# Kernel tuning notes

Hardware: AMD Instinct MI355X
Metric: run time of the kernel (lower is better)

## Reference

```python
import jax, jax.numpy as jnp
import numpy as np

H = 512      # hidden_size
GH = 512     # global_hidden_size
V = 128      # VOCAB_SIZE (one-hot arg_hot width)
D = 14       # tree depth; complete binary tree
NUM_OPS = 36
N_INT = 5    # num_internal_ops
N_NODES = 2 ** (D + 1) - 1  # 32767, heap layout: node i has children 2i+1, 2i+2


def _p(key, i, shape, s=0.05):
    return jax.random.normal(jax.random.fold_in(key, i), shape, dtype=jnp.float32) * s


def setup_inputs() -> dict:
    key = jax.random.key(0)
    return {
        "tokens": jax.random.randint(jax.random.fold_in(key, 0), (N_NODES,), 0, V),
        "validity_mask": jnp.ones((NUM_OPS,), jnp.float32),
        # binary tree-LSTM (blstm): 2 children
        "W_iou_b": _p(key, 1, (V, 3 * H)), "U_iou_b": _p(key, 2, (2, H, 3 * H)), "b_iou_b": jnp.zeros((3 * H,), jnp.float32),
        "Wf_b": _p(key, 3, (V, H)), "Uf_b": _p(key, 4, (2, H, H)), "bf_b": jnp.ones((H,), jnp.float32),
        # ternary tree-LSTM (tlstm): 3 children
        "W_iou_t": _p(key, 5, (V, 3 * H)), "U_iou_t": _p(key, 6, (3, H, 3 * H)), "b_iou_t": jnp.zeros((3 * H,), jnp.float32),
        "Wf_t": _p(key, 7, (V, H)), "Uf_t": _p(key, 8, (3, H, H)), "bf_t": jnp.ones((H,), jnp.float32),
        # FFN: one h-by-h layer (ffn_complexity = h^2 * n_layers, n_layers=1)
        "ffn_W": _p(key, 9, (H, H)), "ffn_b": jnp.zeros((H,), jnp.float32),
        # global LSTM (1 layer, 1 step), torch gate order i,f,g,o
        "lstm_Wx": _p(key, 10, (H, 4 * GH)), "lstm_Wh": _p(key, 11, (GH, 4 * GH)), "lstm_b": jnp.zeros((4 * GH,), jnp.float32),
        # actor heads on concat(root_hidden, h_glob)
        "hl_W": _p(key, 12, (H + GH, 2)), "hl_b": jnp.zeros((2,), jnp.float32),
        "int_W": _p(key, 13, (H + GH, N_INT)), "int_b": jnp.zeros((N_INT,), jnp.float32),
        "act_W": _p(key, 14, (H + GH, NUM_OPS)), "act_b": jnp.zeros((NUM_OPS,), jnp.float32),
    }


def _nary_cell(x, hk, ck, W_iou, U_iou, b_iou, Wf, Uf, bf):
    # x: [n, V]; hk, ck: [n, K, H]  (K children)
    iou = x @ W_iou + jnp.einsum('nkh,khg->ng', hk, U_iou) + b_iou
    i, o, u = jnp.split(iou, 3, axis=-1)
    f = jax.nn.sigmoid((x @ Wf + bf)[:, None, :] + jnp.einsum('nkh,khg->nkg', hk, Uf))
    c = jax.nn.sigmoid(i) * jnp.tanh(u) + jnp.sum(f * ck, axis=1)
    h = jax.nn.sigmoid(o) * jnp.tanh(c)
    return h, c


def _forward(tokens, validity_mask, W_iou_b, U_iou_b, b_iou_b, Wf_b, Uf_b, bf_b,
             W_iou_t, U_iou_t, b_iou_t, Wf_t, Uf_t, bf_t, ffn_W, ffn_b,
             lstm_Wx, lstm_Wh, lstm_b, hl_W, hl_b, int_W, int_b, act_W, act_b):
    arg_hot = jax.nn.one_hot(tokens, V, dtype=jnp.float32)  # [N_NODES, V]
    h_prev = c_prev = None
    h_ab = c_ab = None
    # apply_binary_lstm over the whole tree, bottom-up, one batched cell per level
    for lvl in range(D, -1, -1):
        n = 2 ** lvl
        x = arg_hot[n - 1:2 * n - 1]  # level lvl occupies heap slots [2^l-1, 2^{l+1}-2]
        if h_prev is None:
            hk = jnp.zeros((n, 2, H), jnp.float32)  # leaves: tz children
            ck = hk
        else:
            hk = h_prev.reshape(n, 2, H)
            ck = c_prev.reshape(n, 2, H)
        h_prev, c_prev = _nary_cell(x, hk, ck, W_iou_b, U_iou_b, b_iou_b, Wf_b, Uf_b, bf_b)
        if lvl == 1:
            h_ab, c_ab = h_prev, c_prev  # root's children a, b
    # apply_ternary_lstm at depth 0: children = (self.hidden, a.hidden, b.hidden)
    hk3 = jnp.concatenate([h_prev, h_ab], axis=0)[None]  # [1, 3, H]
    ck3 = jnp.concatenate([c_prev, c_ab], axis=0)[None]
    h_root, c_root = _nary_cell(arg_hot[0:1], hk3, ck3, W_iou_t, U_iou_t, b_iou_t, Wf_t, Uf_t, bf_t)
    # apply_ffn (1 layer) then apply_global_lstm (single step from zero state)
    h_f = jnp.maximum(h_root @ ffn_W + ffn_b, 0.0)  # [1, H]
    h_g = jnp.zeros((1, GH), jnp.float32)
    c_g = h_g
    gates = h_f @ lstm_Wx + h_g @ lstm_Wh + lstm_b
    gi, gf, gg, go = jnp.split(gates, 4, axis=-1)
    c_g = jax.nn.sigmoid(gf) * c_g + jax.nn.sigmoid(gi) * jnp.tanh(gg)
    h_g = jax.nn.sigmoid(go) * jnp.tanh(c_g)
    # actor heads
    feat = jnp.concatenate([h_f, h_g], axis=-1)  # [1, H+GH]
    hl = feat @ hl_W + hl_b
    il = feat @ int_W + int_b
    el = jnp.log(validity_mask)[None, :] + feat @ (act_W * validity_mask[None, :]) + act_b * validity_mask
    return jnp.concatenate([hl, il, el], axis=-1)  # [1, 2 + N_INT + NUM_OPS]


def reference(tokens, validity_mask, W_iou_b, U_iou_b, b_iou_b, Wf_b, Uf_b, bf_b,
              W_iou_t, U_iou_t, b_iou_t, Wf_t, Uf_t, bf_t, ffn_W, ffn_b,
              lstm_Wx, lstm_Wh, lstm_b, hl_W, hl_b, int_W, int_b, act_W, act_b):
    return _forward(tokens, validity_mask, W_iou_b, U_iou_b, b_iou_b, Wf_b, Uf_b, bf_b,
                    W_iou_t, U_iou_t, b_iou_t, Wf_t, Uf_t, bf_t, ffn_W, ffn_b,
                    lstm_Wx, lstm_Wh, lstm_b, hl_W, hl_b, int_W, int_b, act_W, act_b)
```

## Files before the change

### kernel.cpp

```cpp
#include <hip/hip_runtime.h>
#include <hip/hip_bf16.h>
#include <math.h>

#define H 512
#define V 128
#define NLEAF 16384

typedef __attribute__((ext_vector_type(4))) float f32x4;
typedef __attribute__((ext_vector_type(8))) short s16x8;
typedef __attribute__((ext_vector_type(4))) unsigned short u16x4;
typedef unsigned short ushort_t;

__device__ ushort_t g_hb0[NLEAF * H];
__device__ ushort_t g_hb1[(NLEAF / 2) * H];
__device__ float    g_c0[NLEAF * H];
__device__ float    g_c1[(NLEAF / 2) * H];
__device__ ushort_t g_UiouT[3 * H * 2 * H];
__device__ ushort_t g_UfT[H * 2 * H];
__device__ ushort_t g_UiouTt[3 * H * 3 * H];
__device__ ushort_t g_UfTt[H * 3 * H];
__device__ float    g_rpart[3 * 3072];
__device__ float    g_hf[H];
__device__ float    g_gates[4 * H];

__device__ __forceinline__ float sigm(float x) { return 1.0f / (1.0f + __expf(-x)); }
__device__ __forceinline__ float ftanh(float x) {
  return 1.0f - 2.0f / (__expf(2.0f * x) + 1.0f);
}
__device__ __forceinline__ ushort_t f2bf(float x) {
  __hip_bfloat16 b = __float2bfloat16(x);
  return *reinterpret_cast<ushort_t*>(&b);
}
__device__ __forceinline__ float bf2f(ushort_t u) {
  union { unsigned int i; float f; } v; v.i = ((unsigned int)u) << 16; return v.f;
}
__device__ __forceinline__ void gload_lds16(const void* g, void* l) {
  __builtin_amdgcn_global_load_lds(
      (const __attribute__((address_space(1))) unsigned int*)g,
      (__attribute__((address_space(3))) unsigned int*)l, 16, 0, 0);
}

__global__ __launch_bounds__(256) void k_prep(
    const float* __restrict__ s0, const float* __restrict__ s1,
    const float* __restrict__ s2, const float* __restrict__ s3,
    ushort_t* __restrict__ d0, ushort_t* __restrict__ d1,
    ushort_t* __restrict__ d2, ushort_t* __restrict__ d3,
    const int* __restrict__ tokens,
    const float* __restrict__ Wiou, const float* __restrict__ biou) {
  if (blockIdx.z == 4) {
    const int total = NLEAF * 128;
    const int bid = blockIdx.y * 48 + blockIdx.x;
    for (int q = bid * 256 + threadIdx.x; q < total; q += 2304 * 256) {
      int i = q >> 7, jv = q & 127;
      int tok = tokens[(NLEAF - 1) + i];
      const f32x4* Wr = (const f32x4*)(Wiou + (size_t)tok * 1536);
      const f32x4* bv = (const f32x4*)biou;
      f32x4 wi = Wr[jv] + bv[jv];
      f32x4 wo = Wr[128 + jv] + bv[128 + jv];
      f32x4 wu = Wr[256 + jv] + bv[256 + jv];
      u16x4 hv; f32x4 cv;
      #pragma unroll
      for (int r = 0; r < 4; ++r) {
        float c = sigm(wi[r]) * ftanh(wu[r]);
        float h = sigm(wo[r]) * ftanh(c);
        cv[r] = c;
        hv[r] = f2bf(h);
      }
      *reinterpret_cast<u16x4*>(&g_hb0[(size_t)q * 4]) = hv;
      *reinterpret_cast<f32x4*>(&g_c0[(size_t)q * 4]) = cv;
    }
    return;
  }
  const float* src; ushort_t* dst; int R, Cc;
  switch (blockIdx.z) {
    case 0: src = s0; dst = d0; R = 1024; Cc = 1536; break;
    case 1: src = s1; dst = d1; R = 1024; Cc = 512; break;
    case 2: src = s2; dst = d2; R = 1536; Cc = 1536; break;
    default: src = s3; dst = d3; R = 1536; Cc = 512; break;
  }
  int bc = blockIdx.x * 32, br = blockIdx.y * 32;
  if (bc >= Cc || br >= R) return;
  __shared__ float t[32][33];
  int tx = threadIdx.x & 31, ty = threadIdx.x >> 5;
  for (int rr = ty; rr < 32; rr += 8)
    t[rr][tx] = src[(size_t)(br + rr) * Cc + bc + tx];
  __syncthreads();
  for (int rr = ty; rr < 32; rr += 8)
    dst[(size_t)(bc + rr) * R + br + tx] = f2bf(t[tx][rr]);
}

__device__ __forceinline__ void mfma_body(int lvl,
    const int* __restrict__ tokens,
    const float* __restrict__ Wiou, const float* __restrict__ biou,
    const float* __restrict__ Wf, const float* __restrict__ bf) {
  const int n = 1 << lvl;
  const int node0 = n - 1;
  const int outp = lvl & 1;
  const ushort_t* __restrict__ hprev = outp ? g_hb0 : g_hb1;
  const float* __restrict__ cprev = outp ? g_c0 : g_c1;
  ushort_t* __restrict__ hout = outp ? g_hb1 : g_hb0;
  float* __restrict__ cout = outp ? g_c1 : g_c0;

  const int orig = blockIdx.x;
  const int qch = gridDim.x >> 3;
  const int wg = (orig & 7) * qch + (orig >> 3);
  const int i0 = (wg >> 3) * 128;
  const int j0 = (wg & 7) * 64;

  const int tid = threadIdx.x;
  const int lane = tid & 63;
  const int w = tid >> 6;
  const int wry = w >> 1;
  const int cx = w & 1;

  __shared__ f32x4 smemv[3072];
  char* smem = (char*)smemv;

  const char* gp[6];
  unsigned lb[6], lstride[6];
  {
    int kb = (lane >> 4) * 16;
    #pragma unroll
    for (int q = 0; q < 6; ++q) {
      int c = w * 6 + q;
      if (c < 8) {
        int row = i0 + c * 16 + (lane & 15);
        gp[q] = (const char*)hprev + (size_t)row * 2048 + kb;
        lb[q] = c * 1024u;
        lstride[q] = 8192u;
      } else {
        int ct = c - 8;
        int col = ct * 16 + (lane & 15);
        int g = col >> 6, jj = j0 + (col & 63);
        const ushort_t* Ub = (g < 3) ? (g_UiouT + (size_t)(g * 512 + jj) * 1024)
                                     : (g_UfT + (size_t)jj * 1024);
        gp[q] = (const char*)Ub + kb;
        lb[q] = 16384u + ct * 1024u;
        lstride[q] = 16384u;
      }
    }
  }

#define STAGE(BUF)                                                   \
  {                                                                  \
    _Pragma("unroll")                                                \
    for (int q = 0; q < 6; ++q) {                                    \
      gload_lds16(gp[q], smem + lb[q] + (unsigned)(BUF) * lstride[q]); \
      gp[q] += 64;                                                   \
    }                                                                \
  }
#define WAITV(N) asm volatile("s_waitcnt vmcnt(" #N ")" ::: "memory")

  f32x4 acc[4][10];
  #pragma unroll
  for (int a = 0; a < 4; ++a)
    #pragma unroll
    for (int b = 0; b < 10; ++b) acc[a][b] = (f32x4){0.f, 0.f, 0.f, 0.f};

#define COMPUTE(FA)                                                          \
  {                                                                          \
    const char* ab = smem + buf * 8192 + wry * 4096 + lane * 16;             \
    s16x8 a0 = *(const s16x8*)(ab);                                          \
    s16x8 a1 = *(const s16x8*)(ab + 1024);                                   \
    s16x8 a2 = *(const s16x8*)(ab + 2048);                                   \
    s16x8 a3 = *(const s16x8*)(ab + 3072);                                   \
    const char* bb = smem + 16384 + buf * 16384 + cx * 2048 + lane * 16;     \
    s16x8 b0 = *(const s16x8*)(bb);                                          \
    s16x8 b1 = *(const s16x8*)(bb + 1024);                                   \
    s16x8 b2 = *(const s16x8*)(bb + 4096);                                   \
    s16x8 b3 = *(const s16x8*)(bb + 5120);                                   \
    s16x8 b4 = *(const s16x8*)(bb + 8192);                                   \
    s16x8 b5 = *(const s16x8*)(bb + 9216);                                   \
    s16x8 b6 = *(const s16x8*)(bb + 12288);                                  \
    s16x8 b7 = *(const s16x8*)(bb + 13312);                                  \
    s16x8 aa[4] = {a0, a1, a2, a3};                                          \
    _Pragma("unroll")                                                        \
    for (int rtl = 0; rtl < 4; ++rtl) {                                      \
      acc[rtl][0] = __builtin_amdgcn_mfma_f32_16x16x32_bf16(aa[rtl], b0, acc[rtl][0], 0, 0, 0); \
      acc[rtl][1] = __builtin_amdgcn_mfma_f32_16x16x32_bf16(aa[rtl], b1, acc[rtl][1], 0, 0, 0); \
      acc[rtl][2] = __builtin_amdgcn_mfma_f32_16x16x32_bf16(aa[rtl], b2, acc[rtl][2], 0, 0, 0); \
      acc[rtl][3] = __builtin_amdgcn_mfma_f32_16x16x32_bf16(aa[rtl], b3, acc[rtl][3], 0, 0, 0); \
      acc[rtl][4] = __builtin_amdgcn_mfma_f32_16x16x32_bf16(aa[rtl], b4, acc[rtl][4], 0, 0, 0); \
      acc[rtl][5] = __builtin_amdgcn_mfma_f32_16x16x32_bf16(aa[rtl], b5, acc[rtl][5], 0, 0, 0); \
      acc[rtl][FA] = __builtin_amdgcn_mfma_f32_16x16x32_bf16(aa[rtl], b6, acc[rtl][FA], 0, 0, 0); \
      acc[rtl][FA + 1] = __builtin_amdgcn_mfma_f32_16x16x32_bf16(aa[rtl], b7, acc[rtl][FA + 1], 0, 0, 0); \
    }                                                                        \
  }

  STAGE(0); STAGE(1);
  int buf = 0;
  for (int kt = 0; kt < 16; ++kt) {
    WAITV(6);
    __builtin_amdgcn_s_barrier();
    COMPUTE(6);
    __builtin_amdgcn_s_barrier();
    STAGE(buf);
    buf ^= 1;
  }
  for (int kt = 16; kt < 30; ++kt) {
    WAITV(6);
    __builtin_amdgcn_s_barrier();
    COMPUTE(8);
    __builtin_amdgcn_s_barrier();
    STAGE(buf);
    buf ^= 1;
  }
  WAITV(6); __builtin_amdgcn_s_barrier(); COMPUTE(8); buf ^= 1;
  WAITV(0); __builtin_amdgcn_s_barrier(); COMPUTE(8);
#undef COMPUTE
#undef STAGE
#undef WAITV

  const int node_c = lane >> 4;
  const int jl = lane & 15;
  #pragma unroll
  for (int t = 0; t < 2; ++t) {
    const int j = j0 + cx * 32 + t * 16 + jl;
    const float bi = biou[j], bo = biou[512 + j], bu = biou[1024 + j], bfv = bf[j];
    #pragma unroll
    for (int rtl = 0; rtl < 4; ++rtl) {
      f32x4 vi = acc[rtl][0 + t], vo = acc[rtl][2 + t], vu = acc[rtl][4 + t],
            v0 = acc[rtl][6 + t], v1 = acc[rtl][8 + t];
      const int ib = i0 + wry * 64 + rtl * 16 + node_c * 4;
      #pragma unroll
      for (int r = 0; r < 4; ++r) {
        int i = ib + r;
        int tok = tokens[node0 + i];
        const float* Wr = Wiou + (size_t)tok * 1536;
        float fpre = Wf[(size_t)tok * 512 + j] + bfv;
        float ig = vi[r] + Wr[j] + bi;
        float og = vo[r] + Wr[512 + j] + bo;
        float ug = vu[r] + Wr[1024 + j] + bu;
        float cc = sigm(ig) * ftanh(ug)
                 + sigm(fpre + v0[r]) * cprev[(size_t)(2 * i) * 512 + j]
                 + sigm(fpre + v1[r]) * cprev[(size_t)(2 * i + 1) * 512 + j];
        float hh = sigm(og) * ftanh(cc);
        hout[(size_t)i * 512 + j] = f2bf(hh);
        cout[(size_t)i * 512 + j] = cc;
      }
    }
  }
}

__global__ __launch_bounds__(256, 2) void k_mfma_top(
    const int* __restrict__ tokens,
    const float* __restrict__ Wiou, const float* __restrict__ biou,
    const float* __restrict__ Wf, const float* __restrict__ bf) {
  mfma_body(13, tokens, Wiou, biou, Wf, bf);
}
__global__ __launch_bounds__(256, 2) void k_mfma_rest(int lvl,
    const int* __restrict__ tokens,
    const float* __restrict__ Wiou, const float* __restrict__ biou,
    const float* __restrict__ Wf, const float* __restrict__ bf) {
  mfma_body(lvl, tokens, Wiou, biou, Wf, bf);
}

__global__ __launch_bounds__(256) void k_small(int lvl,
    const int* __restrict__ tokens,
    const float* __restrict__ Wiou, const float* __restrict__ biou,
    const float* __restrict__ Wf, const float* __restrict__ bf) {
  const int n = 1 << lvl;
  const int node0 = n - 1;
  const int outp = lvl & 1;
  const ushort_t* __restrict__ hprev = outp ? g_hb0 : g_hb1;
  const float* __restrict__ cprev = outp ? g_c0 : g_c1;
  ushort_t* __restrict__ hout = outp ? g_hb1 : g_hb0;
  float* __restrict__ cout = outp ? g_c1 : g_c0;

  const int i = blockIdx.y;
  const int j0 = blockIdx.x * 64;
  const int tid = threadIdx.x;
  const int g = tid >> 6;
  const int jc = tid & 63;
  const int jj = j0 + jc;

  __shared__ float hl[1024];
  __shared__ float exch[5][64];
  for (int t = tid; t < 1024; t += 256) hl[t] = bf2f(hprev[(size_t)i * 1024 + t]);
  __syncthreads();

  const ushort_t* col = (g < 3) ? (g_UiouT + (size_t)(g * 512 + jj) * 1024)
                                : (g_UfT + (size_t)jj * 1024);
  float a0 = 0.f, a1 = 0.f;
  #pragma unroll 4
  for (int k0 = 0; k0 < 512; k0 += 8) {
    s16x8 wv = *(const s16x8*)(col + k0);
    #pragma unroll
    for (int r = 0; r < 8; ++r) a0 += hl[k0 + r] * bf2f((ushort_t)wv[r]);
  }
  #pragma unroll 4
  for (int k0 = 512; k0 < 1024; k0 += 8) {
    s16x8 wv = *(const s16x8*)(col + k0);
    #pragma unroll
    for (int r = 0; r < 8; ++r) a1 += hl[k0 + r] * bf2f((ushort_t)wv[r]);
  }
  if (g < 3) exch[g][jc] = a0 + a1;
  else { exch[3][jc] = a0; exch[4][jc] = a1; }
  __syncthreads();

  if (tid < 64) {
    int j = j0 + tid;
    float ai = exch[0][tid], ao = exch[1][tid], au = exch[2][tid];
    float af0 = exch[3][tid], af1 = exch[4][tid];
    int tok = tokens[node0 + i];
    const float* Wr = Wiou + (size_t)tok * 1536;
    float fpre = Wf[(size_t)tok * 512 + j] + bf[j];
    float ig = ai + Wr[j] + biou[j];
    float og = ao + Wr[512 + j] + biou[512 + j];
    float ug = au + Wr[1024 + j] + biou[1024 + j];
    float cc = sigm(ig) * ftanh(ug)
             + sigm(fpre + af0) * cprev[(size_t)(2 * i) * 512 + j]
             + sigm(fpre + af1) * cprev[(size_t)(2 * i + 1) * 512 + j];
    float hh = sigm(og) * ftanh(cc);
    hout[(size_t)i * 512 + j] = f2bf(hh);
    cout[(size_t)i * 512 + j] = cc;
  }
}

__global__ __launch_bounds__(256) void k_root_p1() {
  const int by = blockIdx.y;
  const int tid = threadIdx.x;
  const int c = blockIdx.x * 256 + tid;

  __shared__ float hl[512];
  {
    int m0 = by * 512;
    #pragma unroll
    for (int q = 0; q < 2; ++q) {
      int t = tid + q * 256, m = m0 + t;
      hl[t] = (m < 512) ? bf2f(g_hb0[m]) : bf2f(g_hb1[m - 512]);
    }
  }
  __syncthreads();

  float acc = 0.f;
  const ushort_t* col = nullptr;
  if (c < 1536) {
    col = g_UiouTt + (size_t)c * 1536 + by * 512;
  } else {
    int v = c - 1536;
    if ((v >> 9) == by) col = g_UfTt + (size_t)(v & 511) * 1536 + by * 512;
  }
  if (col) {
    #pragma unroll 4
    for (int k0 = 0; k0 < 512; k0 += 8) {
      s16x8 wv = *(const s16x8*)(col + k0);
      #pragma unroll
      for (int r = 0; r < 8; ++r) acc += hl[k0 + r] * bf2f((ushort_t)wv[r]);
    }
  }
  g_rpart[(size_t)by * 3072 + c] = acc;
}

__global__ __launch_bounds__(512) void k_p2h1(const int* __restrict__ tokens,
    const float* __restrict__ Wiou_t, const float* __restrict__ biou_t,
    const float* __restrict__ Wf_t, const float* __restrict__ bf_t,
    const float* __restrict__ ffnW, const float* __restrict__ ffnb) {
  __shared__ float hroot[H];
  const int j = threadIdx.x;
  float ai = g_rpart[j] + g_rpart[3072 + j] + g_rpart[6144 + j];
  float ao = g_rpart[512 + j] + g_rpart[3072 + 512 + j] + g_rpart[6144 + 512 + j];
  float au = g_rpart[1024 + j] + g_rpart[3072 + 1024 + j] + g_rpart[6144 + 1024 + j];
  float f0 = g_rpart[1536 + j] + g_rpart[3072 + 1536 + j] + g_rpart[6144 + 1536 + j];
  float f1 = g_rpart[2048 + j] + g_rpart[3072 + 2048 + j] + g_rpart[6144 + 2048 + j];
  float f2 = g_rpart[2560 + j] + g_rpart[3072 + 2560 + j] + g_rpart[6144 + 2560 + j];

  int tok = tokens[0];
  float fpre = Wf_t[(size_t)tok * H + j] + bf_t[j];
  float ig = ai + Wiou_t[(size_t)tok * 3 * H + j] + biou_t[j];
  float og = ao + Wiou_t[(size_t)tok * 3 * H + H + j] + biou_t[H + j];
  float ug = au + Wiou_t[(size_t)tok * 3 * H + 2 * H + j] + biou_t[2 * H + j];
  float cc = sigm(ig) * ftanh(ug)
           + sigm(fpre + f0) * g_c0[j]
           + sigm(fpre + f1) * g_c1[j]
           + sigm(fpre + f2) * g_c1[H + j];
  hroot[j] = sigm(og) * ftanh(cc);
  __syncthreads();

  float acc = ffnb[j];
  #pragma unroll 8
  for (int m = 0; m < H; ++m) acc += hroot[m] * ffnW[m * H + j];
  g_hf[j] = fmaxf(acc, 0.0f);
}

__global__ __launch_bounds__(64) void k_head2(const float* __restrict__ Wx,
                                              const float* __restrict__ lb) {
  int idx = blockIdx.x * 64 + threadIdx.x;
  int region = idx >> 9;
  int j = idx & 511;
  int g2 = (region == 0) ? j : ((region == 1) ? 1024 + j : 1536 + j);
  float acc = lb[g2];
  #pragma unroll 8
  for (int m = 0; m < H; ++m) acc += g_hf[m] * Wx[m * 4 * H + g2];
  g_gates[g2] = acc;
}

__global__ __launch_bounds__(512) void k_head3(const float* __restrict__ vm,
    const float* __restrict__ hlW, const float* __restrict__ hlb,
    const float* __restrict__ intW, const float* __restrict__ intb,
    const float* __restrict__ actW, const float* __restrict__ actb,
    float* __restrict__ out) {
  __shared__ float feat[2 * H];
  int j = threadIdx.x;
  float ci = sigm(g_gates[j]) * ftanh(g_gates[2 * H + j]);
  float hg = sigm(g_gates[3 * H + j]) * ftanh(ci);
  feat[j] = g_hf[j];
  feat[H + j] = hg;
  __syncthreads();

  const int wv = threadIdx.x >> 6;
  const int lane = threadIdx.x & 63;
  for (int o = wv; o < 43; o += 8) {
    const float* Wc;
    int stride, colb;
    if (o < 2)       { Wc = hlW;  stride = 2;  colb = o; }
    else if (o < 7)  { Wc = intW; stride = 5;  colb = o - 2; }
    else             { Wc = actW; stride = 36; colb = o - 7; }
    float s = 0.f;
    #pragma unroll
    for (int q = 0; q < 16; ++q) {
      int m = lane + q * 64;
      s += feat[m] * Wc[(size_t)m * stride + colb];
    }
    #pragma unroll
    for (int d = 32; d >= 1; d >>= 1) s += __shfl_xor(s, d);
    if (lane == 0) {
      float res;
      if (o < 2)      res = s + hlb[o];
      else if (o < 7) res = s + intb[o - 2];
      else {
        int a = o - 7;
        float v = vm[a];
        res = __logf(v) + s * v + actb[a] * v;
      }
      out[o] = res;
    }
  }
}

extern "C" void kernel_launch(void* const* d_in, const int* in_sizes, int n_in,
                              void* d_out, int out_size, void* d_ws, size_t ws_size,
                              hipStream_t stream) {
  (void)in_sizes; (void)n_in; (void)d_ws; (void)ws_size; (void)out_size;
  const int* tokens   = (const int*)d_in[0];
  const float* vm     = (const float*)d_in[1];
  const float* Wiou_b = (const float*)d_in[2];
  const float* Uiou_b = (const float*)d_in[3];
  const float* biou_b = (const float*)d_in[4];
  const float* Wf_b   = (const float*)d_in[5];
  const float* Uf_b   = (const float*)d_in[6];
  const float* bf_b   = (const float*)d_in[7];
  const float* Wiou_t = (const float*)d_in[8];
  const float* Uiou_t = (const float*)d_in[9];
  const float* biou_t = (const float*)d_in[10];
  const float* Wf_t   = (const float*)d_in[11];
  const float* Uf_t   = (const float*)d_in[12];
  const float* bf_t   = (const float*)d_in[13];
  const float* ffnW   = (const float*)d_in[14];
  const float* ffnb   = (const float*)d_in[15];
  const float* lstmWx = (const float*)d_in[16];
  const float* lstmb  = (const float*)d_in[18];
  const float* hlW    = (const float*)d_in[19];
  const float* hlb    = (const float*)d_in[20];
  const float* intW   = (const float*)d_in[21];
  const float* intb   = (const float*)d_in[22];
  const float* actW   = (const float*)d_in[23];
  const float* actb   = (const float*)d_in[24];

  ushort_t* UiouT;  hipGetSymbolAddress((void**)&UiouT, HIP_SYMBOL(g_UiouT));
  ushort_t* UfT;    hipGetSymbolAddress((void**)&UfT, HIP_SYMBOL(g_UfT));
  ushort_t* UiouTt; hipGetSymbolAddress((void**)&UiouTt, HIP_SYMBOL(g_UiouTt));
  ushort_t* UfTt;   hipGetSymbolAddress((void**)&UfTt, HIP_SYMBOL(g_UfTt));

  k_prep<<<dim3(48, 48, 5), 256, 0, stream>>>(
      Uiou_b, Uf_b, Uiou_t, Uf_t, UiouT, UfT, UiouTt, UfTt,
      tokens, Wiou_b, biou_b);

  k_mfma_top<<<512, 256, 0, stream>>>(tokens, Wiou_b, biou_b, Wf_b, bf_b);
  for (int lvl = 12; lvl >= 8; --lvl) {
    int nb = ((1 << lvl) / 128) * 8;
    k_mfma_rest<<<nb, 256, 0, stream>>>(lvl, tokens, Wiou_b, biou_b,
                                        Wf_b, bf_b);
  }
  for (int lvl = 7; lvl >= 0; --lvl) {
    int n = 1 << lvl;
    k_small<<<dim3(8, n), 256, 0, stream>>>(lvl, tokens, Wiou_b, biou_b,
                                            Wf_b, bf_b);
  }
  k_root_p1<<<dim3(12, 3), 256, 0, stream>>>();
  k_p2h1<<<1, 512, 0, stream>>>(tokens, Wiou_t, biou_t, Wf_t, bf_t, ffnW, ffnb);
  k_head2<<<24, 64, 0, stream>>>(lstmWx, lstmb);
  k_head3<<<1, 512, 0, stream>>>(vm, hlW, hlb, intW, intb, actW, actb, (float*)d_out);
}
```

Before: 670.5 us.

## Replace leaf-state materialization with per-token lookup table and triple-buffer MFMA pipeline

Leaf hidden and cell states depend only on the token, so the code now computes a 128-entry table instead of writing 16384 leaf rows. The top MFMA level gathers its A operand directly from that table by child token, and its epilogue reads the cell state from the table the same way. Both MFMA kernels also move from two-stage to three-stage LDS buffering, raising shared memory to 72KB per block, and use a 2D grid in place of the old swizzled block index. This removes a large leaf write and re-read in exchange for gathered loads, more LDS, and possibly lower occupancy.

```diff
diff --git a/kernel.cpp b/kernel.cpp
--- a/kernel.cpp
+++ b/kernel.cpp
@@ -8,13 +8,14 @@
 
 typedef __attribute__((ext_vector_type(4))) float f32x4;
 typedef __attribute__((ext_vector_type(8))) short s16x8;
-typedef __attribute__((ext_vector_type(4))) unsigned short u16x4;
 typedef unsigned short ushort_t;
 
 __device__ ushort_t g_hb0[NLEAF * H];
 __device__ ushort_t g_hb1[(NLEAF / 2) * H];
 __device__ float    g_c0[NLEAF * H];
 __device__ float    g_c1[(NLEAF / 2) * H];
+__device__ __align__(16) ushort_t g_htab[V * H];
+__device__ __align__(16) float    g_ctab[V * H];
 __device__ ushort_t g_UiouT[3 * H * 2 * H];
 __device__ ushort_t g_UfT[H * 2 * H];
 __device__ ushort_t g_UiouTt[3 * H * 3 * H];
@@ -45,29 +46,18 @@
     const float* __restrict__ s2, const float* __restrict__ s3,
     ushort_t* __restrict__ d0, ushort_t* __restrict__ d1,
     ushort_t* __restrict__ d2, ushort_t* __restrict__ d3,
-    const int* __restrict__ tokens,
     const float* __restrict__ Wiou, const float* __restrict__ biou) {
   if (blockIdx.z == 4) {
-    const int total = NLEAF * 128;
-    const int bid = blockIdx.y * 48 + blockIdx.x;
-    for (int q = bid * 256 + threadIdx.x; q < total; q += 2304 * 256) {
-      int i = q >> 7, jv = q & 127;
-      int tok = tokens[(NLEAF - 1) + i];
-      const f32x4* Wr = (const f32x4*)(Wiou + (size_t)tok * 1536);
-      const f32x4* bv = (const f32x4*)biou;
-      f32x4 wi = Wr[jv] + bv[jv];
-      f32x4 wo = Wr[128 + jv] + bv[128 + jv];
-      f32x4 wu = Wr[256 + jv] + bv[256 + jv];
-      u16x4 hv; f32x4 cv;
-      #pragma unroll
-      for (int r = 0; r < 4; ++r) {
-        float c = sigm(wi[r]) * ftanh(wu[r]);
-        float h = sigm(wo[r]) * ftanh(c);
-        cv[r] = c;
-        hv[r] = f2bf(h);
-      }
-      *reinterpret_cast<u16x4*>(&g_hb0[(size_t)q * 4]) = hv;
-      *reinterpret_cast<f32x4*>(&g_c0[(size_t)q * 4]) = cv;
+    const int v = blockIdx.y * 48 + blockIdx.x;
+    if (v >= V) return;
+    for (int j = threadIdx.x; j < H; j += 256) {
+      float ig = Wiou[(size_t)v * 1536 + j] + biou[j];
+      float og = Wiou[(size_t)v * 1536 + 512 + j] + biou[512 + j];
+      float ug = Wiou[(size_t)v * 1536 + 1024 + j] + biou[1024 + j];
+      float c = sigm(ig) * ftanh(ug);
+      float h = sigm(og) * ftanh(c);
+      g_htab[v * H + j] = f2bf(h);
+      g_ctab[v * H + j] = c;
     }
     return;
   }
@@ -89,82 +79,14 @@
     dst[(size_t)(bc + rr) * R + br + tx] = f2bf(t[tx][rr]);
 }
 
-__device__ __forceinline__ void mfma_body(int lvl,
-    const int* __restrict__ tokens,
-    const float* __restrict__ Wiou, const float* __restrict__ biou,
-    const float* __restrict__ Wf, const float* __restrict__ bf) {
-  const int n = 1 << lvl;
-  const int node0 = n - 1;
-  const int outp = lvl & 1;
-  const ushort_t* __restrict__ hprev = outp ? g_hb0 : g_hb1;
-  const float* __restrict__ cprev = outp ? g_c0 : g_c1;
-  ushort_t* __restrict__ hout = outp ? g_hb1 : g_hb0;
-  float* __restrict__ cout = outp ? g_c1 : g_c0;
-
-  const int orig = blockIdx.x;
-  const int qch = gridDim.x >> 3;
-  const int wg = (orig & 7) * qch + (orig >> 3);
-  const int i0 = (wg >> 3) * 128;
-  const int j0 = (wg & 7) * 64;
-
-  const int tid = threadIdx.x;
-  const int lane = tid & 63;
-  const int w = tid >> 6;
-  const int wry = w >> 1;
-  const int cx = w & 1;
-
-  __shared__ f32x4 smemv[3072];
-  char* smem = (char*)smemv;
-
-  const char* gp[6];
-  unsigned lb[6], lstride[6];
-  {
-    int kb = (lane >> 4) * 16;
-    #pragma unroll
-    for (int q = 0; q < 6; ++q) {
-      int c = w * 6 + q;
-      if (c < 8) {
-        int row = i0 + c * 16 + (lane & 15);
-        gp[q] = (const char*)hprev + (size_t)row * 2048 + kb;
-        lb[q] = c * 1024u;
-        lstride[q] = 8192u;
-      } else {
-        int ct = c - 8;
-        int col = ct * 16 + (lane & 15);
-        int g = col >> 6, jj = j0 + (col & 63);
-        const ushort_t* Ub = (g < 3) ? (g_UiouT + (size_t)(g * 512 + jj) * 1024)
-                                     : (g_UfT + (size_t)jj * 1024);
-        gp[q] = (const char*)Ub + kb;
-        lb[q] = 16384u + ct * 1024u;
-        lstride[q] = 16384u;
-      }
-    }
-  }
-
-#define STAGE(BUF)                                                   \
-  {                                                                  \
-    _Pragma("unroll")                                                \
-    for (int q = 0; q < 6; ++q) {                                    \
-      gload_lds16(gp[q], smem + lb[q] + (unsigned)(BUF) * lstride[q]); \
-      gp[q] += 64;                                                   \
-    }                                                                \
-  }
-#define WAITV(N) asm volatile("s_waitcnt vmcnt(" #N ")" ::: "memory")
-
-  f32x4 acc[4][10];
-  #pragma unroll
-  for (int a = 0; a < 4; ++a)
-    #pragma unroll
-    for (int b = 0; b < 10; ++b) acc[a][b] = (f32x4){0.f, 0.f, 0.f, 0.f};
-
-#define COMPUTE(FA)                                                          \
+#define MFMA_COMPUTE(FA)                                                     \
   {                                                                          \
     const char* ab = smem + buf * 8192 + wry * 4096 + lane * 16;             \
     s16x8 a0 = *(const s16x8*)(ab);                                          \
     s16x8 a1 = *(const s16x8*)(ab + 1024);                                   \
     s16x8 a2 = *(const s16x8*)(ab + 2048);                                   \
     s16x8 a3 = *(const s16x8*)(ab + 3072);                                   \
-    const char* bb = smem + 16384 + buf * 16384 + cx * 2048 + lane * 16;     \
+    const char* bb = smem + 24576 + buf * 16384 + cx * 2048 + lane * 16;     \
     s16x8 b0 = *(const s16x8*)(bb);                                          \
     s16x8 b1 = *(const s16x8*)(bb + 1024);                                   \
     s16x8 b2 = *(const s16x8*)(bb + 4096);                                   \
@@ -186,73 +108,228 @@
       acc[rtl][FA + 1] = __builtin_amdgcn_mfma_f32_16x16x32_bf16(aa[rtl], b7, acc[rtl][FA + 1], 0, 0, 0); \
     }                                                                        \
   }
-
-  STAGE(0); STAGE(1);
-  int buf = 0;
-  for (int kt = 0; kt < 16; ++kt) {
-    WAITV(6);
-    __builtin_amdgcn_s_barrier();
-    COMPUTE(6);
-    __builtin_amdgcn_s_barrier();
-    STAGE(buf);
-    buf ^= 1;
-  }
-  for (int kt = 16; kt < 30; ++kt) {
-    WAITV(6);
-    __builtin_amdgcn_s_barrier();
-    COMPUTE(8);
-    __builtin_amdgcn_s_barrier();
-    STAGE(buf);
-    buf ^= 1;
-  }
-  WAITV(6); __builtin_amdgcn_s_barrier(); COMPUTE(8); buf ^= 1;
-  WAITV(0); __builtin_amdgcn_s_barrier(); COMPUTE(8);
-#undef COMPUTE
-#undef STAGE
-#undef WAITV
-
-  const int node_c = lane >> 4;
-  const int jl = lane & 15;
-  #pragma unroll
-  for (int t = 0; t < 2; ++t) {
-    const int j = j0 + cx * 32 + t * 16 + jl;
-    const float bi = biou[j], bo = biou[512 + j], bu = biou[1024 + j], bfv = bf[j];
-    #pragma unroll
-    for (int rtl = 0; rtl < 4; ++rtl) {
-      f32x4 vi = acc[rtl][0 + t], vo = acc[rtl][2 + t], vu = acc[rtl][4 + t],
-            v0 = acc[rtl][6 + t], v1 = acc[rtl][8 + t];
-      const int ib = i0 + wry * 64 + rtl * 16 + node_c * 4;
-      #pragma unroll
-      for (int r = 0; r < 4; ++r) {
-        int i = ib + r;
-        int tok = tokens[node0 + i];
-        const float* Wr = Wiou + (size_t)tok * 1536;
-        float fpre = Wf[(size_t)tok * 512 + j] + bfv;
-        float ig = vi[r] + Wr[j] + bi;
-        float og = vo[r] + Wr[512 + j] + bo;
-        float ug = vu[r] + Wr[1024 + j] + bu;
-        float cc = sigm(ig) * ftanh(ug)
-                 + sigm(fpre + v0[r]) * cprev[(size_t)(2 * i) * 512 + j]
-                 + sigm(fpre + v1[r]) * cprev[(size_t)(2 * i + 1) * 512 + j];
-        float hh = sigm(og) * ftanh(cc);
-        hout[(size_t)i * 512 + j] = f2bf(hh);
-        cout[(size_t)i * 512 + j] = cc;
-      }
-    }
-  }
-}
+#define WAITV(N) asm volatile("s_waitcnt vmcnt(" #N ")" ::: "memory")
+
+#define MFMA_EPILOGUE(CREAD0, CREAD1)                                        \
+  {                                                                          \
+    const int node_c = lane >> 4;                                            \
+    const int jl = lane & 15;                                                \
+    _Pragma("unroll")                                                        \
+    for (int t = 0; t < 2; ++t) {                                            \
+      const int j = j0 + cx * 32 + t * 16 + jl;                              \
+      const float bi = biou[j], bo = biou[512 + j], bu = biou[1024 + j],     \
+                  bfv = bf[j];                                               \
+      _Pragma("unroll")                                                      \
+      for (int rtl = 0; rtl < 4; ++rtl) {                                    \
+        f32x4 vi = acc[rtl][0 + t], vo = acc[rtl][2 + t],                    \
+              vu = acc[rtl][4 + t], v0 = acc[rtl][6 + t],                    \
+              v1 = acc[rtl][8 + t];                                          \
+        const int ib = i0 + wry * 64 + rtl * 16 + node_c * 4;                \
+        _Pragma("unroll")                                                    \
+        for (int r = 0; r < 4; ++r) {                                        \
+          int i = ib + r;                                                    \
+          int tok = tokens[node0 + i];                                       \
+          const float* Wr = Wiou + (size_t)tok * 1536;                       \
+          float fpre = Wf[(size_t)tok * 512 + j] + bfv;                      \
+          float ig = vi[r] + Wr[j] + bi;                                     \
+          float og = vo[r] + Wr[512 + j] + bo;                               \
+          float ug = vu[r] + Wr[1024 + j] + bu;                              \
+          float cc = sigm(ig) * ftanh(ug)                                    \
+                   + sigm(fpre + v0[r]) * (CREAD0)                           \
+                   + sigm(fpre + v1[r]) * (CREAD1);                          \
+          float hh = sigm(og) * ftanh(cc);                                   \
+          hout[(size_t)i * 512 + j] = f2bf(hh);                              \
+          cout[(size_t)i * 512 + j] = cc;                                    \
+        }                                                                    \
+      }                                                                      \
+    }                                                                        \
+  }
 
 __global__ __launch_bounds__(256, 2) void k_mfma_top(
     const int* __restrict__ tokens,
     const float* __restrict__ Wiou, const float* __restrict__ biou,
     const float* __restrict__ Wf, const float* __restrict__ bf) {
-  mfma_body(13, tokens, Wiou, biou, Wf, bf);
-}
+  const int node0 = 8191;
+  ushort_t* __restrict__ hout = g_hb1;
+  float* __restrict__ cout = g_c1;
+
+  const int i0 = blockIdx.x * 128;
+  const int j0 = blockIdx.y * 64;
+  const int tid = threadIdx.x;
+  const int lane = tid & 63;
+  const int w = tid >> 6;
+  const int wry = w >> 1;
+  const int cx = w & 1;
+
+  __shared__ f32x4 smemv[4608];
+  char* smem = (char*)smemv;
+
+  const char* p0[6]; const char* p1[6];
+  unsigned lb[6], lstr[6], mm[6];
+  {
+    int kb = (lane >> 4) * 16;
+    #pragma unroll
+    for (int q = 0; q < 6; ++q) {
+      int c = w * 6 + q;
+      if (c < 8) {
+        int row = i0 + c * 16 + (lane & 15);
+        int t0 = tokens[(NLEAF - 1) + 2 * row];
+        int t1 = tokens[(NLEAF - 1) + 2 * row + 1];
+        p0[q] = (const char*)g_htab + (size_t)t0 * 1024 + kb;
+        p1[q] = (const char*)g_htab + (size_t)t1 * 1024 + kb;
+        mm[q] = 15u;
+        lb[q] = c * 1024u;
+        lstr[q] = 8192u;
+      } else {
+        int ct = c - 8;
+        int col = ct * 16 + (lane & 15);
+        int g = col >> 6, jj = j0 + (col & 63);
+        const ushort_t* Ub = (g < 3) ? (g_UiouT + (size_t)(g * 512 + jj) * 1024)
+                                     : (g_UfT + (size_t)jj * 1024);
+        p0[q] = (const char*)Ub + kb;
+        p1[q] = p0[q];
+        mm[q] = 63u;
+        lb[q] = 24576u + ct * 1024u;
+        lstr[q] = 16384u;
+      }
+    }
+  }
+
+#define STAGE_T(BUF, SKT)                                                    \
+  {                                                                          \
+    _Pragma("unroll")                                                        \
+    for (int q = 0; q < 6; ++q) {                                            \
+      const char* src = (((SKT) >= 16) ? p1[q] : p0[q]) +                    \
+                        (((unsigned)(SKT) & mm[q]) << 6);                    \
+      gload_lds16(src, smem + lb[q] + (unsigned)(BUF) * lstr[q]);            \
+    }                                                                        \
+  }
+
+  f32x4 acc[4][10];
+  #pragma unroll
+  for (int a = 0; a < 4; ++a)
+    #pragma unroll
+    for (int b = 0; b < 10; ++b) acc[a][b] = (f32x4){0.f, 0.f, 0.f, 0.f};
+
+  STAGE_T(0, 0); STAGE_T(1, 1); STAGE_T(2, 2);
+  int buf = 0;
+  for (int kt = 0; kt < 16; ++kt) {
+    WAITV(12);
+    __builtin_amdgcn_s_barrier();
+    MFMA_COMPUTE(6);
+    __builtin_amdgcn_s_barrier();
+    STAGE_T(buf, kt + 3);
+    buf = (buf == 2) ? 0 : buf + 1;
+  }
+  for (int kt = 16; kt < 29; ++kt) {
+    WAITV(12);
+    __builtin_amdgcn_s_barrier();
+    MFMA_COMPUTE(8);
+    __builtin_amdgcn_s_barrier();
+    STAGE_T(buf, kt + 3);
+    buf = (buf == 2) ? 0 : buf + 1;
+  }
+  WAITV(12); __builtin_amdgcn_s_barrier(); MFMA_COMPUTE(8);
+  buf = (buf == 2) ? 0 : buf + 1;
+  WAITV(6);  __builtin_amdgcn_s_barrier(); MFMA_COMPUTE(8);
+  buf = (buf == 2) ? 0 : buf + 1;
+  WAITV(0);  __builtin_amdgcn_s_barrier(); MFMA_COMPUTE(8);
+#undef STAGE_T
+
+  MFMA_EPILOGUE(g_ctab[(size_t)tokens[(NLEAF - 1) + 2 * i] * 512 + j],
+                g_ctab[(size_t)tokens[(NLEAF - 1) + 2 * i + 1] * 512 + j]);
+}
+
 __global__ __launch_bounds__(256, 2) void k_mfma_rest(int lvl,
     const int* __restrict__ tokens,
     const float* __restrict__ Wiou, const float* __restrict__ biou,
     const float* __restrict__ Wf, const float* __restrict__ bf) {
-  mfma_body(lvl, tokens, Wiou, biou, Wf, bf);
+  const int n = 1 << lvl;
+  const int node0 = n - 1;
+  const int outp = lvl & 1;
+  const ushort_t* __restrict__ hprev = outp ? g_hb0 : g_hb1;
+  const float* __restrict__ cprev = outp ? g_c0 : g_c1;
+  ushort_t* __restrict__ hout = outp ? g_hb1 : g_hb0;
+  float* __restrict__ cout = outp ? g_c1 : g_c0;
+
+  const int i0 = blockIdx.x * 128;
+  const int j0 = blockIdx.y * 64;
+  const int tid = threadIdx.x;
+  const int lane = tid & 63;
+  const int w = tid >> 6;
+  const int wry = w >> 1;
+  const int cx = w & 1;
+
+  __shared__ f32x4 smemv[4608];
+  char* smem = (char*)smemv;
+
+  const char* gp[6];
+  unsigned lb[6], lstr[6];
+  {
+    int kb = (lane >> 4) * 16;
+    #pragma unroll
+    for (int q = 0; q < 6; ++q) {
+      int c = w * 6 + q;
+      if (c < 8) {
+        int row = i0 + c * 16 + (lane & 15);
+        gp[q] = (const char*)hprev + (size_t)row * 2048 + kb;
+        lb[q] = c * 1024u;
+        lstr[q] = 8192u;
+      } else {
+        int ct = c - 8;
+        int col = ct * 16 + (lane & 15);
+        int g = col >> 6, jj = j0 + (col & 63);
+        const ushort_t* Ub = (g < 3) ? (g_UiouT + (size_t)(g * 512 + jj) * 1024)
+                                     : (g_UfT + (size_t)jj * 1024);
+        gp[q] = (const char*)Ub + kb;
+        lb[q] = 24576u + ct * 1024u;
+        lstr[q] = 16384u;
+      }
+    }
+  }
+
+#define STAGE_R(BUF)                                                 \
+  {                                                                  \
+    _Pragma("unroll")                                                \
+    for (int q = 0; q < 6; ++q) {                                    \
+      gload_lds16(gp[q], smem + lb[q] + (unsigned)(BUF) * lstr[q]);  \
+      gp[q] += 64;                                                   \
+    }                                                                \
+  }
+
+  f32x4 acc[4][10];
+  #pragma unroll
+  for (int a = 0; a < 4; ++a)
+    #pragma unroll
+    for (int b = 0; b < 10; ++b) acc[a][b] = (f32x4){0.f, 0.f, 0.f, 0.f};
+
+  STAGE_R(0); STAGE_R(1); STAGE_R(2);
+  int buf = 0;
+  for (int kt = 0; kt < 16; ++kt) {
+    WAITV(12);
+    __builtin_amdgcn_s_barrier();
+    MFMA_COMPUTE(6);
+    __builtin_amdgcn_s_barrier();
+    STAGE_R(buf);
+    buf = (buf == 2) ? 0 : buf + 1;
+  }
+  for (int kt = 16; kt < 29; ++kt) {
+    WAITV(12);
+    __builtin_amdgcn_s_barrier();
+    MFMA_COMPUTE(8);
+    __builtin_amdgcn_s_barrier();
+    STAGE_R(buf);
+    buf = (buf == 2) ? 0 : buf + 1;
+  }
+  WAITV(12); __builtin_amdgcn_s_barrier(); MFMA_COMPUTE(8);
+  buf = (buf == 2) ? 0 : buf + 1;
+  WAITV(6);  __builtin_amdgcn_s_barrier(); MFMA_COMPUTE(8);
+  buf = (buf == 2) ? 0 : buf + 1;
+  WAITV(0);  __builtin_amdgcn_s_barrier(); MFMA_COMPUTE(8);
+#undef STAGE_R
+
+  MFMA_EPILOGUE(cprev[(size_t)(2 * i) * 512 + j],
+                cprev[(size_t)(2 * i + 1) * 512 + j]);
 }
 
 __global__ __launch_bounds__(256) void k_small(int lvl,
@@ -473,14 +550,14 @@
   ushort_t* UfTt;   hipGetSymbolAddress((void**)&UfTt, HIP_SYMBOL(g_UfTt));
 
   k_prep<<<dim3(48, 48, 5), 256, 0, stream>>>(
-      Uiou_b, Uf_b, Uiou_t, Uf_t, UiouT, UfT, UiouTt, UfTt,
-      tokens, Wiou_b, biou_b);
-
-  k_mfma_top<<<512, 256, 0, stream>>>(tokens, Wiou_b, biou_b, Wf_b, bf_b);
+      Uiou_b, Uf_b, Uiou_t, Uf_t, UiouT, UfT, UiouTt, UfTt, Wiou_b, biou_b);
+
+  k_mfma_top<<<dim3(64, 8), 256, 0, stream>>>(tokens, Wiou_b, biou_b,
+                                              Wf_b, bf_b);
   for (int lvl = 12; lvl >= 8; --lvl) {
-    int nb = ((1 << lvl) / 128) * 8;
-    k_mfma_rest<<<nb, 256, 0, stream>>>(lvl, tokens, Wiou_b, biou_b,
-                                        Wf_b, bf_b);
+    int gx = (1 << lvl) / 128;
+    k_mfma_rest<<<dim3(gx, 8), 256, 0, stream>>>(lvl, tokens, Wiou_b, biou_b,
+                                                 Wf_b, bf_b);
   }
   for (int lvl = 7; lvl >= 0; --lvl) {
     int n = 1 << lvl;
```

Result: faster. 584.7 us (-12.8%).

## Precompute per-token leaf states and child projections to skip level-13 GEMM

Applied to the files above, without the earlier changes.

Leaves depend only on their token, so leaf h and c are tabulated per vocabulary entry, and the children's U projections are precomputed per token (128×3584 GEMV). Level 13 then becomes a gather-and-elementwise kernel instead of a large MFMA GEMM. The MFMA kernel also moves to a 3-stage LDS pipeline with a 2D grid, and the W/bias terms are packed into one float4 table. This removes most of the largest GEMM level at the cost of extra small kernels, more LDS per block, and bf16 rounding of leaf h before the precompute.

```diff
diff --git a/kernel.cpp b/kernel.cpp
--- a/kernel.cpp
+++ b/kernel.cpp
@@ -15,6 +15,13 @@
 __device__ ushort_t g_hb1[(NLEAF / 2) * H];
 __device__ float    g_c0[NLEAF * H];
 __device__ float    g_c1[(NLEAF / 2) * H];
+__device__ __align__(16) ushort_t g_htab[V * H];
+__device__ __align__(16) float    g_ctab[V * H];
+__device__ __align__(16) float    g_Wpack[V * H * 4];
+__device__ __align__(16) float    g_Uh0[V * 3 * H];
+__device__ __align__(16) float    g_Uh1[V * 3 * H];
+__device__ __align__(16) float    g_Vf0[V * H];
+__device__ __align__(16) float    g_Vf1[V * H];
 __device__ ushort_t g_UiouT[3 * H * 2 * H];
 __device__ ushort_t g_UfT[H * 2 * H];
 __device__ ushort_t g_UiouTt[3 * H * 3 * H];
@@ -45,29 +52,22 @@
     const float* __restrict__ s2, const float* __restrict__ s3,
     ushort_t* __restrict__ d0, ushort_t* __restrict__ d1,
     ushort_t* __restrict__ d2, ushort_t* __restrict__ d3,
-    const int* __restrict__ tokens,
-    const float* __restrict__ Wiou, const float* __restrict__ biou) {
+    const float* __restrict__ Wiou, const float* __restrict__ biou,
+    const float* __restrict__ Wf, const float* __restrict__ bf) {
   if (blockIdx.z == 4) {
-    const int total = NLEAF * 128;
-    const int bid = blockIdx.y * 48 + blockIdx.x;
-    for (int q = bid * 256 + threadIdx.x; q < total; q += 2304 * 256) {
-      int i = q >> 7, jv = q & 127;
-      int tok = tokens[(NLEAF - 1) + i];
-      const f32x4* Wr = (const f32x4*)(Wiou + (size_t)tok * 1536);
-      const f32x4* bv = (const f32x4*)biou;
-      f32x4 wi = Wr[jv] + bv[jv];
-      f32x4 wo = Wr[128 + jv] + bv[128 + jv];
-      f32x4 wu = Wr[256 + jv] + bv[256 + jv];
-      u16x4 hv; f32x4 cv;
-      #pragma unroll
-      for (int r = 0; r < 4; ++r) {
-        float c = sigm(wi[r]) * ftanh(wu[r]);
-        float h = sigm(wo[r]) * ftanh(c);
-        cv[r] = c;
-        hv[r] = f2bf(h);
-      }
-      *reinterpret_cast<u16x4*>(&g_hb0[(size_t)q * 4]) = hv;
-      *reinterpret_cast<f32x4*>(&g_c0[(size_t)q * 4]) = cv;
+    const int v = blockIdx.y * 48 + blockIdx.x;
+    if (v >= V) return;
+    for (int j = threadIdx.x; j < H; j += 256) {
+      float wi = Wiou[(size_t)v * 1536 + j] + biou[j];
+      float wo = Wiou[(size_t)v * 1536 + 512 + j] + biou[512 + j];
+      float wu = Wiou[(size_t)v * 1536 + 1024 + j] + biou[1024 + j];
+      float wf = Wf[(size_t)v * 512 + j] + bf[j];
+      f32x4 wp = {wi, wo, wu, wf};
+      *reinterpret_cast<f32x4*>(&g_Wpack[((size_t)v * 512 + j) * 4]) = wp;
+      float c = sigm(wi) * ftanh(wu);
+      float h = sigm(wo) * ftanh(c);
+      g_htab[v * H + j] = f2bf(h);
+      g_ctab[v * H + j] = c;
     }
     return;
   }
@@ -89,82 +89,75 @@
     dst[(size_t)(bc + rr) * R + br + tx] = f2bf(t[tx][rr]);
 }
 
-__device__ __forceinline__ void mfma_body(int lvl,
-    const int* __restrict__ tokens,
-    const float* __restrict__ Wiou, const float* __restrict__ biou,
-    const float* __restrict__ Wf, const float* __restrict__ bf) {
-  const int n = 1 << lvl;
-  const int node0 = n - 1;
-  const int outp = lvl & 1;
-  const ushort_t* __restrict__ hprev = outp ? g_hb0 : g_hb1;
-  const float* __restrict__ cprev = outp ? g_c0 : g_c1;
-  ushort_t* __restrict__ hout = outp ? g_hb1 : g_hb0;
-  float* __restrict__ cout = outp ? g_c1 : g_c0;
-
-  const int orig = blockIdx.x;
-  const int qch = gridDim.x >> 3;
-  const int wg = (orig & 7) * qch + (orig >> 3);
-  const int i0 = (wg >> 3) * 128;
-  const int j0 = (wg & 7) * 64;
-
-  const int tid = threadIdx.x;
-  const int lane = tid & 63;
-  const int w = tid >> 6;
-  const int wry = w >> 1;
-  const int cx = w & 1;
-
-  __shared__ f32x4 smemv[3072];
-  char* smem = (char*)smemv;
-
-  const char* gp[6];
-  unsigned lb[6], lstride[6];
-  {
-    int kb = (lane >> 4) * 16;
-    #pragma unroll
-    for (int q = 0; q < 6; ++q) {
-      int c = w * 6 + q;
-      if (c < 8) {
-        int row = i0 + c * 16 + (lane & 15);
-        gp[q] = (const char*)hprev + (size_t)row * 2048 + kb;
-        lb[q] = c * 1024u;
-        lstride[q] = 8192u;
-      } else {
-        int ct = c - 8;
-        int col = ct * 16 + (lane & 15);
-        int g = col >> 6, jj = j0 + (col & 63);
-        const ushort_t* Ub = (g < 3) ? (g_UiouT + (size_t)(g * 512 + jj) * 1024)
-                                     : (g_UfT + (size_t)jj * 1024);
-        gp[q] = (const char*)Ub + kb;
-        lb[q] = 16384u + ct * 1024u;
-        lstride[q] = 16384u;
-      }
-    }
-  }
-
-#define STAGE(BUF)                                                   \
-  {                                                                  \
-    _Pragma("unroll")                                                \
-    for (int q = 0; q < 6; ++q) {                                    \
-      gload_lds16(gp[q], smem + lb[q] + (unsigned)(BUF) * lstride[q]); \
-      gp[q] += 64;                                                   \
-    }                                                                \
-  }
-#define WAITV(N) asm volatile("s_waitcnt vmcnt(" #N ")" ::: "memory")
-
-  f32x4 acc[4][10];
-  #pragma unroll
-  for (int a = 0; a < 4; ++a)
-    #pragma unroll
-    for (int b = 0; b < 10; ++b) acc[a][b] = (f32x4){0.f, 0.f, 0.f, 0.f};
-
-#define COMPUTE(FA)                                                          \
+__global__ __launch_bounds__(256) void k_uh() {
+  const int v = blockIdx.x;
+  const int c = blockIdx.y * 256 + threadIdx.x;
+  __shared__ float hl[512];
+  for (int t = threadIdx.x; t < 512; t += 256) hl[t] = bf2f(g_htab[v * 512 + t]);
+  __syncthreads();
+  const ushort_t* col; float* dst;
+  if (c < 1536)      { col = g_UiouT + (size_t)c * 1024;
+                       dst = &g_Uh0[(size_t)v * 1536 + c]; }
+  else if (c < 3072) { col = g_UiouT + (size_t)(c - 1536) * 1024 + 512;
+                       dst = &g_Uh1[(size_t)v * 1536 + (c - 1536)]; }
+  else if (c < 3584) { col = g_UfT + (size_t)(c - 3072) * 1024;
+                       dst = &g_Vf0[(size_t)v * 512 + (c - 3072)]; }
+  else               { col = g_UfT + (size_t)(c - 3584) * 1024 + 512;
+                       dst = &g_Vf1[(size_t)v * 512 + (c - 3584)]; }
+  float acc = 0.f;
+  #pragma unroll 4
+  for (int k0 = 0; k0 < 512; k0 += 8) {
+    s16x8 wv = *(const s16x8*)(col + k0);
+    #pragma unroll
+    for (int r = 0; r < 8; ++r) acc += hl[k0 + r] * bf2f((ushort_t)wv[r]);
+  }
+  *dst = acc;
+}
+
+__global__ __launch_bounds__(256) void k_top_cell(const int* __restrict__ tokens) {
+  const int total = 8192 * 128;
+  for (int q = blockIdx.x * 256 + threadIdx.x; q < total; q += gridDim.x * 256) {
+    int i = q >> 7, jv = q & 127;
+    int t0 = tokens[(NLEAF - 1) + 2 * i];
+    int t1 = tokens[(NLEAF - 1) + 2 * i + 1];
+    int tk = tokens[8191 + i];
+    const f32x4* u0 = (const f32x4*)&g_Uh0[(size_t)t0 * 1536];
+    const f32x4* u1 = (const f32x4*)&g_Uh1[(size_t)t1 * 1536];
+    f32x4 ii = u0[jv] + u1[jv];
+    f32x4 oo = u0[128 + jv] + u1[128 + jv];
+    f32x4 uu = u0[256 + jv] + u1[256 + jv];
+    f32x4 v0 = ((const f32x4*)&g_Vf0[(size_t)t0 * 512])[jv];
+    f32x4 v1 = ((const f32x4*)&g_Vf1[(size_t)t1 * 512])[jv];
+    f32x4 c0 = ((const f32x4*)&g_ctab[(size_t)t0 * 512])[jv];
+    f32x4 c1 = ((const f32x4*)&g_ctab[(size_t)t1 * 512])[jv];
+    const f32x4* wpp = (const f32x4*)g_Wpack + (size_t)tk * 512 + jv * 4;
+    u16x4 hv; f32x4 cv;
+    #pragma unroll
+    for (int r = 0; r < 4; ++r) {
+      f32x4 wp = wpp[r];
+      float ig = ii[r] + wp[0];
+      float og = oo[r] + wp[1];
+      float ug = uu[r] + wp[2];
+      float fp = wp[3];
+      float cc = sigm(ig) * ftanh(ug) + sigm(fp + v0[r]) * c0[r]
+               + sigm(fp + v1[r]) * c1[r];
+      float hh = sigm(og) * ftanh(cc);
+      cv[r] = cc;
+      hv[r] = f2bf(hh);
+    }
+    *reinterpret_cast<u16x4*>(&g_hb1[(size_t)q * 4]) = hv;
+    *reinterpret_cast<f32x4*>(&g_c1[(size_t)q * 4]) = cv;
+  }
+}
+
+#define MFMA_COMPUTE(FA)                                                     \
   {                                                                          \
     const char* ab = smem + buf * 8192 + wry * 4096 + lane * 16;             \
     s16x8 a0 = *(const s16x8*)(ab);                                          \
     s16x8 a1 = *(const s16x8*)(ab + 1024);                                   \
     s16x8 a2 = *(const s16x8*)(ab + 2048);                                   \
     s16x8 a3 = *(const s16x8*)(ab + 3072);                                   \
-    const char* bb = smem + 16384 + buf * 16384 + cx * 2048 + lane * 16;     \
+    const char* bb = smem + 24576 + buf * 16384 + cx * 2048 + lane * 16;     \
     s16x8 b0 = *(const s16x8*)(bb);                                          \
     s16x8 b1 = *(const s16x8*)(bb + 1024);                                   \
     s16x8 b2 = *(const s16x8*)(bb + 4096);                                   \
@@ -186,37 +179,99 @@
       acc[rtl][FA + 1] = __builtin_amdgcn_mfma_f32_16x16x32_bf16(aa[rtl], b7, acc[rtl][FA + 1], 0, 0, 0); \
     }                                                                        \
   }
-
-  STAGE(0); STAGE(1);
+#define WAITV(N) asm volatile("s_waitcnt vmcnt(" #N ")" ::: "memory")
+
+__global__ __launch_bounds__(256, 2) void k_mfma_rest(int lvl,
+    const int* __restrict__ tokens) {
+  const int n = 1 << lvl;
+  const int node0 = n - 1;
+  const int outp = lvl & 1;
+  const ushort_t* __restrict__ hprev = outp ? g_hb0 : g_hb1;
+  const float* __restrict__ cprev = outp ? g_c0 : g_c1;
+  ushort_t* __restrict__ hout = outp ? g_hb1 : g_hb0;
+  float* __restrict__ cout = outp ? g_c1 : g_c0;
+
+  const int i0 = blockIdx.x * 128;
+  const int j0 = blockIdx.y * 64;
+  const int tid = threadIdx.x;
+  const int lane = tid & 63;
+  const int w = tid >> 6;
+  const int wry = w >> 1;
+  const int cx = w & 1;
+
+  __shared__ f32x4 smemv[4608];
+  char* smem = (char*)smemv;
+
+  const char* gp[6];
+  unsigned lb[6], lstr[6];
+  {
+    int kb = (lane >> 4) * 16;
+    #pragma unroll
+    for (int q = 0; q < 6; ++q) {
+      int c = w * 6 + q;
+      if (c < 8) {
+        int row = i0 + c * 16 + (lane & 15);
+        gp[q] = (const char*)hprev + (size_t)row * 2048 + kb;
+        lb[q] = c * 1024u;
+        lstr[q] = 8192u;
+      } else {
+        int ct = c - 8;
+        int col = ct * 16 + (lane & 15);
+        int g = col >> 6, jj = j0 + (col & 63);
+        const ushort_t* Ub = (g < 3) ? (g_UiouT + (size_t)(g * 512 + jj) * 1024)
+                                     : (g_UfT + (size_t)jj * 1024);
+        gp[q] = (const char*)Ub + kb;
+        lb[q] = 24576u + ct * 1024u;
+        lstr[q] = 16384u;
+      }
+    }
+  }
+
+#define STAGE_R(BUF)                                                 \
+  {                                                                  \
+    _Pragma("unroll")                                                \
+    for (int q = 0; q < 6; ++q) {                                    \
+      gload_lds16(gp[q], smem + lb[q] + (unsigned)(BUF) * lstr[q]);  \
+      gp[q] += 64;                                                   \
+    }                                                                \
+  }
+
+  f32x4 acc[4][10];
+  #pragma unroll
+  for (int a = 0; a < 4; ++a)
+    #pragma unroll
+    for (int b = 0; b < 10; ++b) acc[a][b] = (f32x4){0.f, 0.f, 0.f, 0.f};
+
+  STAGE_R(0); STAGE_R(1); STAGE_R(2);
   int buf = 0;
   for (int kt = 0; kt < 16; ++kt) {
-    WAITV(6);
+    WAITV(12);
     __builtin_amdgcn_s_barrier();
-    COMPUTE(6);
+    MFMA_COMPUTE(6);
     __builtin_amdgcn_s_barrier();
-    STAGE(buf);
-    buf ^= 1;
-  }
-  for (int kt = 16; kt < 30; ++kt) {
-    WAITV(6);
+    STAGE_R(buf);
+    buf = (buf == 2) ? 0 : buf + 1;
+  }
+  for (int kt = 16; kt < 29; ++kt) {
+    WAITV(12);
     __builtin_amdgcn_s_barrier();
-    COMPUTE(8);
+    MFMA_COMPUTE(8);
     __builtin_amdgcn_s_barrier();
-    STAGE(buf);
-    buf ^= 1;
-  }
-  WAITV(6); __builtin_amdgcn_s_barrier(); COMPUTE(8); buf ^= 1;
-  WAITV(0); __builtin_amdgcn_s_barrier(); COMPUTE(8);
-#undef COMPUTE
-#undef STAGE
-#undef WAITV
+    STAGE_R(buf);
+    buf = (buf == 2) ? 0 : buf + 1;
+  }
+  WAITV(12); __builtin_amdgcn_s_barrier(); MFMA_COMPUTE(8);
+  buf = (buf == 2) ? 0 : buf + 1;
+  WAITV(6);  __builtin_amdgcn_s_barrier(); MFMA_COMPUTE(8);
+  buf = (buf == 2) ? 0 : buf + 1;
+  WAITV(0);  __builtin_amdgcn_s_barrier(); MFMA_COMPUTE(8);
+#undef STAGE_R
 
   const int node_c = lane >> 4;
   const int jl = lane & 15;
   #pragma unroll
   for (int t = 0; t < 2; ++t) {
     const int j = j0 + cx * 32 + t * 16 + jl;
-    const float bi = biou[j], bo = biou[512 + j], bu = biou[1024 + j], bfv = bf[j];
     #pragma unroll
     for (int rtl = 0; rtl < 4; ++rtl) {
       f32x4 vi = acc[rtl][0 + t], vo = acc[rtl][2 + t], vu = acc[rtl][4 + t],
@@ -226,11 +281,11 @@
       for (int r = 0; r < 4; ++r) {
         int i = ib + r;
         int tok = tokens[node0 + i];
-        const float* Wr = Wiou + (size_t)tok * 1536;
-        float fpre = Wf[(size_t)tok * 512 + j] + bfv;
-        float ig = vi[r] + Wr[j] + bi;
-        float og = vo[r] + Wr[512 + j] + bo;
-        float ug = vu[r] + Wr[1024 + j] + bu;
+        f32x4 wp = ((const f32x4*)g_Wpack)[(size_t)tok * 512 + j];
+        float ig = vi[r] + wp[0];
+        float og = vo[r] + wp[1];
+        float ug = vu[r] + wp[2];
+        float fpre = wp[3];
         float cc = sigm(ig) * ftanh(ug)
                  + sigm(fpre + v0[r]) * cprev[(size_t)(2 * i) * 512 + j]
                  + sigm(fpre + v1[r]) * cprev[(size_t)(2 * i + 1) * 512 + j];
@@ -242,23 +297,8 @@
   }
 }
 
-__global__ __launch_bounds__(256, 2) void k_mfma_top(
-    const int* __restrict__ tokens,
-    const float* __restrict__ Wiou, const float* __restrict__ biou,
-    const float* __restrict__ Wf, const float* __restrict__ bf) {
-  mfma_body(13, tokens, Wiou, biou, Wf, bf);
-}
-__global__ __launch_bounds__(256, 2) void k_mfma_rest(int lvl,
-    const int* __restrict__ tokens,
-    const float* __restrict__ Wiou, const float* __restrict__ biou,
-    const float* __restrict__ Wf, const float* __restrict__ bf) {
-  mfma_body(lvl, tokens, Wiou, biou, Wf, bf);
-}
-
 __global__ __launch_bounds__(256) void k_small(int lvl,
-    const int* __restrict__ tokens,
-    const float* __restrict__ Wiou, const float* __restrict__ biou,
-    const float* __restrict__ Wf, const float* __restrict__ bf) {
+    const int* __restrict__ tokens) {
   const int n = 1 << lvl;
   const int node0 = n - 1;
   const int outp = lvl & 1;
@@ -300,17 +340,15 @@
 
   if (tid < 64) {
     int j = j0 + tid;
-    float ai = exch[0][tid], ao = exch[1][tid], au = exch[2][tid];
-    float af0 = exch[3][tid], af1 = exch[4][tid];
     int tok = tokens[node0 + i];
-    const float* Wr = Wiou + (size_t)tok * 1536;
-    float fpre = Wf[(size_t)tok * 512 + j] + bf[j];
-    float ig = ai + Wr[j] + biou[j];
-    float og = ao + Wr[512 + j] + biou[512 + j];
-    float ug = au + Wr[1024 + j] + biou[1024 + j];
+    f32x4 wp = ((const f32x4*)g_Wpack)[(size_t)tok * 512 + j];
+    float ig = exch[0][tid] + wp[0];
+    float og = exch[1][tid] + wp[1];
+    float ug = exch[2][tid] + wp[2];
+    float fpre = wp[3];
     float cc = sigm(ig) * ftanh(ug)
-             + sigm(fpre + af0) * cprev[(size_t)(2 * i) * 512 + j]
-             + sigm(fpre + af1) * cprev[(size_t)(2 * i + 1) * 512 + j];
+             + sigm(fpre + exch[3][tid]) * cprev[(size_t)(2 * i) * 512 + j]
+             + sigm(fpre + exch[4][tid]) * cprev[(size_t)(2 * i + 1) * 512 + j];
     float hh = sigm(og) * ftanh(cc);
     hout[(size_t)i * 512 + j] = f2bf(hh);
     cout[(size_t)i * 512 + j] = cc;
@@ -474,18 +512,18 @@
 
   k_prep<<<dim3(48, 48, 5), 256, 0, stream>>>(
       Uiou_b, Uf_b, Uiou_t, Uf_t, UiouT, UfT, UiouTt, UfTt,
-      tokens, Wiou_b, biou_b);
-
-  k_mfma_top<<<512, 256, 0, stream>>>(tokens, Wiou_b, biou_b, Wf_b, bf_b);
+      Wiou_b, biou_b, Wf_b, bf_b);
+
+  k_uh<<<dim3(128, 16), 256, 0, stream>>>();
+  k_top_cell<<<2048, 256, 0, stream>>>(tokens);
+
   for (int lvl = 12; lvl >= 8; --lvl) {
-    int nb = ((1 << lvl) / 128) * 8;
-    k_mfma_rest<<<nb, 256, 0, stream>>>(lvl, tokens, Wiou_b, biou_b,
-                                        Wf_b, bf_b);
+    int gx = (1 << lvl) / 128;
+    k_mfma_rest<<<dim3(gx, 8), 256, 0, stream>>>(lvl, tokens);
   }
   for (int lvl = 7; lvl >= 0; --lvl) {
     int n = 1 << lvl;
-    k_small<<<dim3(8, n), 256, 0, stream>>>(lvl, tokens, Wiou_b, biou_b,
-                                            Wf_b, bf_b);
+    k_small<<<dim3(8, n), 256, 0, stream>>>(lvl, tokens);
   }
   k_root_p1<<<dim3(12, 3), 256, 0, stream>>>();
   k_p2h1<<<1, 512, 0, stream>>>(tokens, Wiou_t, biou_t, Wf_t, bf_t, ffnW, ffnb);
```

Result: faster. 606.4 us (-9.6%).
